# Kernel tuning notes

Hardware: AMD Instinct MI355X
Metric: run time of the kernel (lower is better)

Reference implementation:

```python
import jax, jax.numpy as jnp
import numpy as np

E = 1_000_000
N = 100_000
D = 128            # node/edge feature dim
H = 128            # hidden dim
CIN = 3 * D        # concat(efeat, src_nfeat, dst_nfeat)
EPS = 1e-5


def setup_inputs() -> dict:
    key = jax.random.key(0)
    ks = jax.random.split(key, 10)
    scale = 1.0 / np.sqrt(CIN)
    return {
        "efeat": jax.random.normal(ks[0], (E, D), dtype=jnp.float32),
        "nfeat": jax.random.normal(ks[1], (N, D), dtype=jnp.float32),
        "src_idx": jax.random.randint(ks[2], (E,), 0, N, dtype=jnp.int32),
        "dst_idx": jax.random.randint(ks[3], (E,), 0, N, dtype=jnp.int32),
        "W1": jax.random.normal(ks[4], (CIN, H), dtype=jnp.float32) * scale,
        "b1": jnp.zeros((H,), dtype=jnp.float32),
        "W2": jax.random.normal(ks[5], (H, D), dtype=jnp.float32) * (1.0 / np.sqrt(H)),
        "b2": jnp.zeros((D,), dtype=jnp.float32),
        "ln_g": jnp.ones((D,), dtype=jnp.float32),
        "ln_b": jnp.zeros((D,), dtype=jnp.float32),
    }


def _layernorm(x, g, b):
    mu = jnp.mean(x, axis=-1, keepdims=True)
    var = jnp.var(x, axis=-1, keepdims=True)
    return (x - mu) * jax.lax.rsqrt(var + EPS) * g + b


def reference(efeat, nfeat, src_idx, dst_idx, W1, b1, W2, b2, ln_g, ln_b):
    # gather source/target node feats and concat with edge feats: [E, 3D]
    cat = jnp.concatenate([efeat, nfeat[src_idx], nfeat[dst_idx]], axis=-1)
    h = jax.nn.silu(cat @ W1 + b1)            # [E, H]
    out = _layernorm(h @ W2 + b2, ln_g, ln_b)  # [E, D]
    return (out + efeat, nfeat)
```

## Files before the change

### kernel.cpp

```cpp
#include <hip/hip_runtime.h>
#include <cstdint>
#include <cstddef>

#define EE 1000000
#define NN 100000

typedef unsigned short u16;
typedef __bf16 bf16x8 __attribute__((ext_vector_type(8)));
typedef float f32x4 __attribute__((ext_vector_type(4)));

__device__ __forceinline__ u16 f2bf(float f) {
    union { float f; uint32_t u; } v; v.f = f;
    uint32_t r = v.u + 0x7FFFu + ((v.u >> 16) & 1u);
    return (u16)(r >> 16);
}
__device__ __forceinline__ uint32_t f2bf2(float lo, float hi) {
    return (uint32_t)f2bf(lo) | ((uint32_t)f2bf(hi) << 16);
}

__global__ void pack_weights_k(const float* __restrict__ W1, const float* __restrict__ W2,
                               u16* __restrict__ pack) {
    int t = blockIdx.x * 256 + threadIdx.x;
    if (t < 49152) {
        int j = t & 7, lane = (t >> 3) & 63, ct = (t >> 9) & 7, ks = t >> 12;
        int k = ks * 32 + ((lane >> 4) << 3) + j;
        int col = (ct << 4) + (lane & 15);
        pack[t] = f2bf(W1[k * 128 + col]);
    } else if (t < 65536) {
        int u = t - 49152;
        int j = u & 7, lane = (u >> 3) & 63, ct = (u >> 9) & 7, ks = u >> 12;
        int k = ks * 32 + ((lane >> 4) << 3) + j;
        int col = (ct << 4) + (lane & 15);
        pack[t] = f2bf(W2[k * 128 + col]);
    }
}

__global__ void copy_nfeat_k(const float4* __restrict__ s, float4* __restrict__ d, int n) {
    for (int i = blockIdx.x * blockDim.x + threadIdx.x; i < n; i += gridDim.x * blockDim.x)
        d[i] = s[i];
}

__launch_bounds__(512, 2)
__global__ void edge_mlp_k(const float* __restrict__ efeat, const float* __restrict__ nfeat,
                           const int* __restrict__ srci, const int* __restrict__ dsti,
                           const u16* __restrict__ pack,
                           const float* __restrict__ b1p, const float* __restrict__ b2p,
                           const float* __restrict__ gp, const float* __restrict__ bp,
                           float* __restrict__ out) {
    extern __shared__ char smem[];
    u16* w1 = (u16*)smem;
    u16* cbuf = (u16*)(smem + 98304);
    float* lnbuf = (float*)(smem + 98304);

    const int tid = threadIdx.x;
    const int lane = tid & 63;
    const int wid = tid >> 6;
    const int wr = wid >> 1;
    const int wc = wid & 1;

    {
        const uint4* g = (const uint4*)pack;
        uint4* l = (uint4*)smem;
#pragma unroll
        for (int i = 0; i < 12; i++) l[tid + i * 512] = g[tid + i * 512];
    }
    bf16x8 w2f[4][4];
    {
        const bf16x8* g = (const bf16x8*)(pack + 49152);
#pragma unroll
        for (int ks = 0; ks < 4; ks++)
#pragma unroll
            for (int ct = 0; ct < 4; ct++)
                w2f[ks][ct] = g[(ks * 8 + wc * 4 + ct) * 64 + lane];
    }
    float b1v[4], b2v[4], gv[4], bv[4];
#pragma unroll
    for (int ct = 0; ct < 4; ct++) {
        int col = wc * 64 + ct * 16 + (lane & 15);
        b1v[ct] = b1p[col]; b2v[ct] = b2p[col]; gv[ct] = gp[col]; bv[ct] = bp[col];
    }
    __syncthreads();

    const int srow = tid & 127;
    const int skc = tid >> 7;

    const int numTiles = (EE + 127) >> 7;
    for (int tile = blockIdx.x; tile < numTiles; tile += gridDim.x) {
        const int base = tile << 7;
        int e_s = base + srow; if (e_s >= EE) e_s = EE - 1;
        const int sn = srci[e_s];
        const int dn = dsti[e_s];
        const float* rowp[3];
        rowp[0] = efeat + (size_t)e_s * 128;
        rowp[1] = nfeat + (size_t)sn * 128;
        rowp[2] = nfeat + (size_t)dn * 128;

        f32x4 acc1[2][4] = {};
        float4 L0, L1, L2, L3;

#define SLOAD(c) { const float4* p4_ = (const float4*)(rowp[(c) >> 1] + (((c) & 1) * 64 + skc * 16)); \
        L0 = p4_[0]; L1 = p4_[1]; L2 = p4_[2]; L3 = p4_[3]; }

#define SWRITE(ci) { u16* buf_ = cbuf + ((ci) & 1) * 8192; \
        int rt_ = srow >> 4; \
        uint4 q0_, q1_; \
        q0_.x = f2bf2(L0.x, L0.y); q0_.y = f2bf2(L0.z, L0.w); \
        q0_.z = f2bf2(L1.x, L1.y); q0_.w = f2bf2(L1.z, L1.w); \
        q1_.x = f2bf2(L2.x, L2.y); q1_.y = f2bf2(L2.z, L2.w); \
        q1_.z = f2bf2(L3.x, L3.y); q1_.w = f2bf2(L3.z, L3.w); \
        int kk0_ = skc * 2; \
        int ksl0_ = kk0_ >> 2;      int la0_ = (srow & 15) + ((kk0_ & 3) << 4); \
        int ksl1_ = (kk0_ + 1) >> 2; int la1_ = (srow & 15) + (((kk0_ + 1) & 3) << 4); \
        *(uint4*)(buf_ + ((rt_ * 2 + ksl0_) * 64 + la0_) * 8) = q0_; \
        *(uint4*)(buf_ + ((rt_ * 2 + ksl1_) * 64 + la1_) * 8) = q1_; }

#define GCHUNK(c, ci) { const u16* buf_ = cbuf + ((ci) & 1) * 8192; \
        _Pragma("unroll") \
        for (int ksl = 0; ksl < 2; ksl++) { \
            int ks_ = (c) * 2 + ksl; \
            bf16x8 a0_ = *(const bf16x8*)(buf_ + (((wr * 2 + 0) * 2 + ksl) * 64 + lane) * 8); \
            bf16x8 a1_ = *(const bf16x8*)(buf_ + (((wr * 2 + 1) * 2 + ksl) * 64 + lane) * 8); \
            _Pragma("unroll") \
            for (int ct = 0; ct < 4; ct++) { \
                bf16x8 b_ = *(const bf16x8*)(w1 + ((ks_ * 8 + wc * 4 + ct) * 64 + lane) * 8); \
                acc1[0][ct] = __builtin_amdgcn_mfma_f32_16x16x32_bf16(a0_, b_, acc1[0][ct], 0, 0, 0); \
                acc1[1][ct] = __builtin_amdgcn_mfma_f32_16x16x32_bf16(a1_, b_, acc1[1][ct], 0, 0, 0); \
            } } }

        SLOAD(2); SWRITE(0);
        __syncthreads();
        SLOAD(3); GCHUNK(2, 0); SWRITE(1); __syncthreads();
        SLOAD(4); GCHUNK(3, 1); SWRITE(2); __syncthreads();
        SLOAD(5); GCHUNK(4, 2); SWRITE(3); __syncthreads();
        SLOAD(0); GCHUNK(5, 3); SWRITE(4); __syncthreads();
        SLOAD(1); GCHUNK(0, 4); SWRITE(5); __syncthreads();
        GCHUNK(1, 5); __syncthreads();

#pragma unroll
        for (int rtl = 0; rtl < 2; rtl++) {
            int rt = wr * 2 + rtl;
#pragma unroll
            for (int ct = 0; ct < 4; ct++) {
                int ks = wc * 2 + (ct >> 1);
                int lahi = ((ct & 1) * 2) + ((lane & 15) >> 3);
                int j = lane & 7;
#pragma unroll
                for (int r = 0; r < 4; r++) {
                    float x = acc1[rtl][ct][r] + b1v[ct];
                    float s = x / (1.f + __expf(-x));
                    int la = ((lane >> 4) * 4 + r) + (lahi << 4);
                    cbuf[((rt * 4 + ks) * 64 + la) * 8 + j] = f2bf(s);
                }
            }
        }
        __syncthreads();

        f32x4 acc2[2][4] = {};
#pragma unroll
        for (int ks2 = 0; ks2 < 4; ks2++) {
            bf16x8 a0 = *(const bf16x8*)(cbuf + (((wr * 2 + 0) * 4 + ks2) * 64 + lane) * 8);
            bf16x8 a1 = *(const bf16x8*)(cbuf + (((wr * 2 + 1) * 4 + ks2) * 64 + lane) * 8);
#pragma unroll
            for (int ct = 0; ct < 4; ct++) {
                acc2[0][ct] = __builtin_amdgcn_mfma_f32_16x16x32_bf16(a0, w2f[ks2][ct], acc2[0][ct], 0, 0, 0);
                acc2[1][ct] = __builtin_amdgcn_mfma_f32_16x16x32_bf16(a1, w2f[ks2][ct], acc2[1][ct], 0, 0, 0);
            }
        }
        __syncthreads();

#pragma unroll
        for (int rtl = 0; rtl < 2; rtl++) {
#pragma unroll
            for (int r = 0; r < 4; r++) {
                float s = 0.f, q = 0.f;
#pragma unroll
                for (int ct = 0; ct < 4; ct++) {
                    float x = acc2[rtl][ct][r] + b2v[ct];
                    s += x; q += x * x;
                }
#pragma unroll
                for (int m = 1; m < 16; m <<= 1) { s += __shfl_xor(s, m); q += __shfl_xor(q, m); }
                if ((lane & 15) == 0) {
                    int row = wr * 32 + rtl * 16 + (lane >> 4) * 4 + r;
                    lnbuf[row * 4 + wc * 2 + 0] = s;
                    lnbuf[row * 4 + wc * 2 + 1] = q;
                }
            }
        }
        __syncthreads();

#pragma unroll
        for (int rtl = 0; rtl < 2; rtl++) {
#pragma unroll
            for (int r = 0; r < 4; r++) {
                int row = wr * 32 + rtl * 16 + (lane >> 4) * 4 + r;
                int e = base + row;
                float mean = (lnbuf[row * 4 + 0] + lnbuf[row * 4 + 2]) * (1.f / 128.f);
                float msq  = (lnbuf[row * 4 + 1] + lnbuf[row * 4 + 3]) * (1.f / 128.f);
                float rstd = rsqrtf(msq - mean * mean + 1e-5f);
                if (e < EE) {
                    const float* ef = efeat + (size_t)e * 128;
                    float* op = out + (size_t)e * 128;
#pragma unroll
                    for (int ct = 0; ct < 4; ct++) {
                        int col = wc * 64 + ct * 16 + (lane & 15);
                        float x = acc2[rtl][ct][r] + b2v[ct];
                        op[col] = (x - mean) * rstd * gv[ct] + bv[ct] + ef[col];
                    }
                }
            }
        }
        __syncthreads();
#undef SLOAD
#undef SWRITE
#undef GCHUNK
    }
}

extern "C" void kernel_launch(void* const* d_in, const int* in_sizes, int n_in,
                              void* d_out, int out_size, void* d_ws, size_t ws_size,
                              hipStream_t stream) {
    const float* efeat = (const float*)d_in[0];
    const float* nfeat = (const float*)d_in[1];
    const int* srci = (const int*)d_in[2];
    const int* dsti = (const int*)d_in[3];
    const float* W1 = (const float*)d_in[4];
    const float* b1 = (const float*)d_in[5];
    const float* W2 = (const float*)d_in[6];
    const float* b2 = (const float*)d_in[7];
    const float* lng = (const float*)d_in[8];
    const float* lnb = (const float*)d_in[9];
    float* out = (float*)d_out;

    u16* pack = (ws_size >= 131072) ? (u16*)d_ws : (u16*)(out + (size_t)EE * 128);

    hipFuncSetAttribute(reinterpret_cast<const void*>(edge_mlp_k),
                        hipFuncAttributeMaxDynamicSharedMemorySize, 131072);

    pack_weights_k<<<256, 256, 0, stream>>>(W1, W2, pack);
    edge_mlp_k<<<256, 512, 131072, stream>>>(efeat, nfeat, srci, dsti, pack,
                                             b1, b2, lng, lnb, out);
    copy_nfeat_k<<<2048, 256, 0, stream>>>((const float4*)nfeat,
                                           (float4*)(out + (size_t)EE * 128),
                                           (NN * 128) / 4);
}
```

Measured before the change: 615.3 us.

## Software-pipeline gathers across tiles, prefetch efeat residual, use lighter barriers

Restructures the edge MLP main loop so the next tile's index loads and first source-node gather are issued during the current tile's compute, and the efeat residual values are held in registers during the GEMMs instead of being reloaded at the epilogue. The feature chunks are reordered (src, dst, efeat) and staged in a two-slot LDS buffer. Layernorm partial sums move to a separate LDS region, which removes one barrier. __syncthreads is replaced with a raw s_barrier plus an lgkmcnt wait, and bf16 conversion uses the native cast. This adds register pressure (efr array and prefetch registers), slightly more LDS, and drops the 2-blocks-per-CU launch-bounds hint.

```diff
diff --git a/kernel.cpp b/kernel.cpp
--- a/kernel.cpp
+++ b/kernel.cpp
@@ -14,8 +14,10 @@
     uint32_t r = v.u + 0x7FFFu + ((v.u >> 16) & 1u);
     return (u16)(r >> 16);
 }
-__device__ __forceinline__ uint32_t f2bf2(float lo, float hi) {
-    return (uint32_t)f2bf(lo) | ((uint32_t)f2bf(hi) << 16);
+__device__ __forceinline__ uint32_t cvt2(float lo, float hi) {
+    u16 a = __builtin_bit_cast(u16, (__bf16)lo);
+    u16 b = __builtin_bit_cast(u16, (__bf16)hi);
+    return (uint32_t)a | ((uint32_t)b << 16);
 }
 
 __global__ void pack_weights_k(const float* __restrict__ W1, const float* __restrict__ W2,
@@ -40,17 +42,21 @@
         d[i] = s[i];
 }
 
-__launch_bounds__(512, 2)
-__global__ void edge_mlp_k(const float* __restrict__ efeat, const float* __restrict__ nfeat,
-                           const int* __restrict__ srci, const int* __restrict__ dsti,
-                           const u16* __restrict__ pack,
-                           const float* __restrict__ b1p, const float* __restrict__ b2p,
-                           const float* __restrict__ gp, const float* __restrict__ bp,
-                           float* __restrict__ out) {
+#define BAR() { asm volatile("s_waitcnt lgkmcnt(0)" ::: "memory"); \
+                __builtin_amdgcn_s_barrier(); \
+                asm volatile("" ::: "memory"); }
+
+__global__ void __launch_bounds__(512)
+edge_mlp_k(const float* __restrict__ efeat, const float* __restrict__ nfeat,
+           const int* __restrict__ srci, const int* __restrict__ dsti,
+           const u16* __restrict__ pack,
+           const float* __restrict__ b1p, const float* __restrict__ b2p,
+           const float* __restrict__ gp, const float* __restrict__ bp,
+           float* __restrict__ out) {
     extern __shared__ char smem[];
     u16* w1 = (u16*)smem;
-    u16* cbuf = (u16*)(smem + 98304);
-    float* lnbuf = (float*)(smem + 98304);
+    u16* bbuf = (u16*)(smem + 98304);
+    float* lnbuf = (float*)(smem + 131072);
 
     const int tid = threadIdx.x;
     const int lane = tid & 63;
@@ -83,38 +89,20 @@
 
     const int srow = tid & 127;
     const int skc = tid >> 7;
-
+    const int G = (int)gridDim.x << 7;
     const int numTiles = (EE + 127) >> 7;
-    for (int tile = blockIdx.x; tile < numTiles; tile += gridDim.x) {
-        const int base = tile << 7;
-        int e_s = base + srow; if (e_s >= EE) e_s = EE - 1;
-        const int sn = srci[e_s];
-        const int dn = dsti[e_s];
-        const float* rowp[3];
-        rowp[0] = efeat + (size_t)e_s * 128;
-        rowp[1] = nfeat + (size_t)sn * 128;
-        rowp[2] = nfeat + (size_t)dn * 128;
-
-        f32x4 acc1[2][4] = {};
-        float4 L0, L1, L2, L3;
-
-#define SLOAD(c) { const float4* p4_ = (const float4*)(rowp[(c) >> 1] + (((c) & 1) * 64 + skc * 16)); \
-        L0 = p4_[0]; L1 = p4_[1]; L2 = p4_[2]; L3 = p4_[3]; }
-
-#define SWRITE(ci) { u16* buf_ = cbuf + ((ci) & 1) * 8192; \
-        int rt_ = srow >> 4; \
+
+#define SWRITE(kb, V0, V1, V2, V3) { u16* buf_ = bbuf + (kb) * 8192; int rt_ = srow >> 4; \
         uint4 q0_, q1_; \
-        q0_.x = f2bf2(L0.x, L0.y); q0_.y = f2bf2(L0.z, L0.w); \
-        q0_.z = f2bf2(L1.x, L1.y); q0_.w = f2bf2(L1.z, L1.w); \
-        q1_.x = f2bf2(L2.x, L2.y); q1_.y = f2bf2(L2.z, L2.w); \
-        q1_.z = f2bf2(L3.x, L3.y); q1_.w = f2bf2(L3.z, L3.w); \
+        q0_.x = cvt2(V0.x, V0.y); q0_.y = cvt2(V0.z, V0.w); \
+        q0_.z = cvt2(V1.x, V1.y); q0_.w = cvt2(V1.z, V1.w); \
+        q1_.x = cvt2(V2.x, V2.y); q1_.y = cvt2(V2.z, V2.w); \
+        q1_.z = cvt2(V3.x, V3.y); q1_.w = cvt2(V3.z, V3.w); \
         int kk0_ = skc * 2; \
-        int ksl0_ = kk0_ >> 2;      int la0_ = (srow & 15) + ((kk0_ & 3) << 4); \
-        int ksl1_ = (kk0_ + 1) >> 2; int la1_ = (srow & 15) + (((kk0_ + 1) & 3) << 4); \
-        *(uint4*)(buf_ + ((rt_ * 2 + ksl0_) * 64 + la0_) * 8) = q0_; \
-        *(uint4*)(buf_ + ((rt_ * 2 + ksl1_) * 64 + la1_) * 8) = q1_; }
-
-#define GCHUNK(c, ci) { const u16* buf_ = cbuf + ((ci) & 1) * 8192; \
+        *(uint4*)(buf_ + ((rt_ * 2 + (kk0_ >> 2)) * 64 + (srow & 15) + ((kk0_ & 3) << 4)) * 8) = q0_; \
+        *(uint4*)(buf_ + ((rt_ * 2 + ((kk0_ + 1) >> 2)) * 64 + (srow & 15) + (((kk0_ + 1) & 3) << 4)) * 8) = q1_; }
+
+#define GCHUNK(c, kb) { const u16* buf_ = bbuf + (kb) * 8192; \
         _Pragma("unroll") \
         for (int ksl = 0; ksl < 2; ksl++) { \
             int ks_ = (c) * 2 + ksl; \
@@ -127,14 +115,79 @@
                 acc1[1][ct] = __builtin_amdgcn_mfma_f32_16x16x32_bf16(a1_, b_, acc1[1][ct], 0, 0, 0); \
             } } }
 
-        SLOAD(2); SWRITE(0);
-        __syncthreads();
-        SLOAD(3); GCHUNK(2, 0); SWRITE(1); __syncthreads();
-        SLOAD(4); GCHUNK(3, 1); SWRITE(2); __syncthreads();
-        SLOAD(5); GCHUNK(4, 2); SWRITE(3); __syncthreads();
-        SLOAD(0); GCHUNK(5, 3); SWRITE(4); __syncthreads();
-        SLOAD(1); GCHUNK(0, 4); SWRITE(5); __syncthreads();
-        GCHUNK(1, 5); __syncthreads();
+#define LD16(P, OFF, V0, V1, V2, V3) { const float4* p_ = (const float4*)((P) + (OFF)); \
+        V0 = p_[0]; V1 = p_[1]; V2 = p_[2]; V3 = p_[3]; }
+
+    int tile = blockIdx.x;
+    {
+        int e0 = (tile << 7) + srow; if (e0 >= EE) e0 = EE - 1;
+        int sn = srci[e0], dn = dsti[e0];
+        (void)sn; (void)dn;
+    }
+    int e0 = (tile << 7) + srow; if (e0 >= EE) e0 = EE - 1;
+    int sn0 = srci[e0], dn0 = dsti[e0];
+    const float* rp0 = efeat + (size_t)e0 * 128;
+    const float* rp1 = nfeat + (size_t)sn0 * 128;
+    const float* rp2 = nfeat + (size_t)dn0 * 128;
+
+    float4 A0, A1, A2, A3, B0, B1, B2, B3;
+    LD16(rp1, 0 + skc * 16, A0, A1, A2, A3);
+    LD16(rp1, 64 + skc * 16, B0, B1, B2, B3);
+
+    for (; tile < numTiles; tile += (int)gridDim.x) {
+        const int base = tile << 7;
+        const bool hasN = (tile + (int)gridDim.x) < numTiles;
+        f32x4 acc1[2][4] = {};
+
+        SWRITE(0, A0, A1, A2, A3);
+        BAR();
+        LD16(rp2, 0 + skc * 16, A0, A1, A2, A3);
+        GCHUNK(2, 0);
+
+        SWRITE(1, B0, B1, B2, B3);
+        BAR();
+        LD16(rp2, 64 + skc * 16, B0, B1, B2, B3);
+        GCHUNK(3, 1);
+
+        SWRITE(0, A0, A1, A2, A3);
+        BAR();
+        int e_n = base + G + srow; if (e_n >= EE) e_n = EE - 1;
+        int sn_n = 0, dn_n = 0;
+        if (hasN) { sn_n = srci[e_n]; dn_n = dsti[e_n]; }
+        float efr[2][4][4];
+#pragma unroll
+        for (int rtl = 0; rtl < 2; rtl++)
+#pragma unroll
+            for (int r = 0; r < 4; r++) {
+                int row = wr * 32 + rtl * 16 + (lane >> 4) * 4 + r;
+                int e = base + row; if (e >= EE) e = EE - 1;
+                const float* ef = efeat + (size_t)e * 128;
+#pragma unroll
+                for (int ct = 0; ct < 4; ct++)
+                    efr[rtl][r][ct] = ef[wc * 64 + ct * 16 + (lane & 15)];
+            }
+        LD16(rp0, 0 + skc * 16, A0, A1, A2, A3);
+        GCHUNK(4, 0);
+
+        SWRITE(1, B0, B1, B2, B3);
+        BAR();
+        LD16(rp0, 64 + skc * 16, B0, B1, B2, B3);
+        GCHUNK(5, 1);
+
+        SWRITE(0, A0, A1, A2, A3);
+        BAR();
+        const float* np0 = efeat + (size_t)e_n * 128;
+        const float* np1 = nfeat + (size_t)sn_n * 128;
+        const float* np2 = nfeat + (size_t)dn_n * 128;
+        if (hasN) LD16(np1, 0 + skc * 16, A0, A1, A2, A3);
+        GCHUNK(0, 0);
+
+        SWRITE(1, B0, B1, B2, B3);
+        BAR();
+        if (hasN) LD16(np1, 64 + skc * 16, B0, B1, B2, B3);
+        GCHUNK(1, 1);
+
+        BAR();
 
 #pragma unroll
         for (int rtl = 0; rtl < 2; rtl++) {
@@ -149,24 +202,23 @@
                     float x = acc1[rtl][ct][r] + b1v[ct];
                     float s = x / (1.f + __expf(-x));
                     int la = ((lane >> 4) * 4 + r) + (lahi << 4);
-                    cbuf[((rt * 4 + ks) * 64 + la) * 8 + j] = f2bf(s);
-                }
-            }
-        }
-        __syncthreads();
+                    bbuf[((rt * 4 + ks) * 64 + la) * 8 + j] = __builtin_bit_cast(u16, (__bf16)s);
+                }
+            }
+        }
+        BAR();
 
         f32x4 acc2[2][4] = {};
 #pragma unroll
         for (int ks2 = 0; ks2 < 4; ks2++) {
-            bf16x8 a0 = *(const bf16x8*)(cbuf + (((wr * 2 + 0) * 4 + ks2) * 64 + lane) * 8);
-            bf16x8 a1 = *(const bf16x8*)(cbuf + (((wr * 2 + 1) * 4 + ks2) * 64 + lane) * 8);
+            bf16x8 a0 = *(const bf16x8*)(bbuf + (((wr * 2 + 0) * 4 + ks2) * 64 + lane) * 8);
+            bf16x8 a1 = *(const bf16x8*)(bbuf + (((wr * 2 + 1) * 4 + ks2) * 64 + lane) * 8);
 #pragma unroll
             for (int ct = 0; ct < 4; ct++) {
                 acc2[0][ct] = __builtin_amdgcn_mfma_f32_16x16x32_bf16(a0, w2f[ks2][ct], acc2[0][ct], 0, 0, 0);
                 acc2[1][ct] = __builtin_amdgcn_mfma_f32_16x16x32_bf16(a1, w2f[ks2][ct], acc2[1][ct], 0, 0, 0);
             }
         }
-        __syncthreads();
 
 #pragma unroll
         for (int rtl = 0; rtl < 2; rtl++) {
@@ -187,7 +239,7 @@
                 }
             }
         }
-        __syncthreads();
+        BAR();
 
 #pragma unroll
         for (int rtl = 0; rtl < 2; rtl++) {
@@ -199,22 +251,22 @@
                 float msq  = (lnbuf[row * 4 + 1] + lnbuf[row * 4 + 3]) * (1.f / 128.f);
                 float rstd = rsqrtf(msq - mean * mean + 1e-5f);
                 if (e < EE) {
-                    const float* ef = efeat + (size_t)e * 128;
                     float* op = out + (size_t)e * 128;
 #pragma unroll
                     for (int ct = 0; ct < 4; ct++) {
                         int col = wc * 64 + ct * 16 + (lane & 15);
                         float x = acc2[rtl][ct][r] + b2v[ct];
-                        op[col] = (x - mean) * rstd * gv[ct] + bv[ct] + ef[col];
+                        op[col] = (x - mean) * rstd * gv[ct] + bv[ct] + efr[rtl][r][ct];
                     }
                 }
             }
         }
-        __syncthreads();
-#undef SLOAD
+
+        rp0 = np0; rp1 = np1; rp2 = np2;
+    }
 #undef SWRITE
 #undef GCHUNK
-    }
+#undef LD16
 }
 
 extern "C" void kernel_launch(void* const* d_in, const int* in_sizes, int n_in,
@@ -235,10 +287,10 @@
     u16* pack = (ws_size >= 131072) ? (u16*)d_ws : (u16*)(out + (size_t)EE * 128);
 
     hipFuncSetAttribute(reinterpret_cast<const void*>(edge_mlp_k),
-                        hipFuncAttributeMaxDynamicSharedMemorySize, 131072);
+                        hipFuncAttributeMaxDynamicSharedMemorySize, 133120);
 
     pack_weights_k<<<256, 256, 0, stream>>>(W1, W2, pack);
-    edge_mlp_k<<<256, 512, 131072, stream>>>(efeat, nfeat, srci, dsti, pack,
+    edge_mlp_k<<<256, 512, 133120, stream>>>(efeat, nfeat, srci, dsti, pack,
                                              b1, b2, lng, lnb, out);
     copy_nfeat_k<<<2048, 256, 0, stream>>>((const float4*)nfeat,
                                            (float4*)(out + (size_t)EE * 128),
```

Measured after the change: 661.3 us. +7.5%, slower.
